# Kernel tuning notes

Measured on AMD Instinct MI355X. Metric: run time of the kernel, lower is better.

The kernel has to match this reference:

```python
import jax, jax.numpy as jnp
import numpy as np

D_MODEL = 1024
NUM_HEADS = 16
MAX_SEQ_LEN = 2048
BATCH = 4
SEQ_LEN = 2048


def setup_inputs() -> dict:
    key = jax.random.key(0)
    ks = jax.random.split(key, 7)
    s = 0.02
    return {
        "x": jax.random.normal(ks[0], (BATCH, SEQ_LEN, D_MODEL), dtype=jnp.float32),
        "Wq": jax.random.normal(ks[1], (D_MODEL, D_MODEL), dtype=jnp.float32) * s,
        "Wk": jax.random.normal(ks[2], (D_MODEL, D_MODEL), dtype=jnp.float32) * s,
        "Wv": jax.random.normal(ks[3], (D_MODEL, D_MODEL), dtype=jnp.float32) * s,
        "Wo": jax.random.normal(ks[4], (D_MODEL, D_MODEL), dtype=jnp.float32) * s,
        "bo": jnp.zeros((D_MODEL,), dtype=jnp.float32),
        "bias_table": jax.random.normal(ks[5], (2 * MAX_SEQ_LEN - 1, NUM_HEADS), dtype=jnp.float32) * s,
    }


def reference(x, Wq, Wk, Wv, Wo, bo, bias_table):
    B, S, D = x.shape
    H = NUM_HEADS
    hd = D // H
    scale = hd ** -0.5

    # torch Linear: y = x @ W.T
    q = (x @ Wq.T).reshape(B, S, H, hd).transpose(0, 2, 1, 3)  # [B,H,S,hd]
    k = (x @ Wk.T).reshape(B, S, H, hd).transpose(0, 2, 1, 3)
    v = (x @ Wv.T).reshape(B, S, H, hd).transpose(0, 2, 1, 3)

    scores = jnp.einsum("bhqd,bhkd->bhqk", q, k) * scale  # [B,H,S,S]

    # relative index: coords[:,None] - coords[None,:] + max_seq_len - 1
    coords = jnp.arange(S)
    rel_idx = coords[:, None] - coords[None, :] + MAX_SEQ_LEN - 1  # [S,S]
    rel_bias = bias_table[rel_idx]              # [S,S,H]
    rel_bias = rel_bias.transpose(2, 0, 1)[None]  # [1,H,S,S]

    probs = jax.nn.softmax(scores + rel_bias, axis=-1)
    ctx = jnp.einsum("bhqk,bhkd->bhqd", probs, v)  # [B,H,S,hd]
    ctx = ctx.transpose(0, 2, 1, 3).reshape(B, S, D)
    return ctx @ Wo.T + bo
```

## Files before the change

### kernel.cpp

```cpp
#include <hip/hip_runtime.h>
#include <string.h>

typedef unsigned short u16;
typedef unsigned int   u32;
typedef __attribute__((ext_vector_type(8))) short short8;
typedef __attribute__((ext_vector_type(4))) float f32x4;
typedef __attribute__((ext_vector_type(16))) float f32x16;
typedef __attribute__((ext_vector_type(2))) __fp16 h2;
typedef __attribute__((ext_vector_type(8))) __fp16 h8;
typedef __attribute__((ext_vector_type(2))) unsigned int u32x2;

__device__ __forceinline__ u16 f2b(float f) {
  u32 u = __float_as_uint(f);
  u32 r = (u + 0x7fffu + ((u >> 16) & 1u)) >> 16;
  return (u16)r;
}
__device__ __forceinline__ void cp16(const u16* g, u16* l) {
  __builtin_amdgcn_global_load_lds(
      (const __attribute__((address_space(1))) void*)g,
      (__attribute__((address_space(3))) void*)l, 16, 0, 0);
}
__device__ __forceinline__ void plswap(u32& a, u32& b) {
  u32x2 r = __builtin_amdgcn_permlane32_swap(a, b, false, false);
  a = r[0]; b = r[1];
}

__global__ __launch_bounds__(256) void cvt_f2b_kernel(const float* __restrict__ in,
                                                      u16* __restrict__ out, int n) {
  int i = (blockIdx.x * 256 + threadIdx.x) * 4;
  if (i + 3 < n) {
    float4 v = *(const float4*)&in[i];
    ushort4 o = make_ushort4(f2b(v.x), f2b(v.y), f2b(v.z), f2b(v.w));
    *(ushort4*)&out[i] = o;
  }
}
__global__ __launch_bounds__(256) void cvtw_kernel(const float* __restrict__ w0,
                                                   const float* __restrict__ w1,
                                                   const float* __restrict__ w2,
                                                   const float* __restrict__ w3,
                                                   u16* __restrict__ out) {
  const float* src = (blockIdx.y == 0) ? w0 : (blockIdx.y == 1) ? w1
                   : (blockIdx.y == 2) ? w2 : w3;
  int i = (blockIdx.x * 256 + threadIdx.x) * 4;
  float4 v = *(const float4*)&src[i];
  ushort4 o = make_ushort4(f2b(v.x), f2b(v.y), f2b(v.z), f2b(v.w));
  *(ushort4*)&out[(size_t)blockIdx.y * 1048576 + i] = o;
}

__global__ __launch_bounds__(256) void bias4x_kernel(const float* __restrict__ bt,
                                                     f32x4* __restrict__ gb4) {
  int idx = blockIdx.x * 256 + threadIdx.x;
  int h = idx >> 12, j = idx & 4095;
  f32x4 v;
  #pragma unroll
  for (int e = 0; e < 4; ++e) {
    int r = j - 3 + e;
    r = r < 0 ? 0 : (r > 4094 ? 4094 : r);
    v[e] = bt[r * 16 + h] * 1.44269504f;
  }
  gb4[idx] = v;
}

template<int MODE>
__global__ __launch_bounds__(256) void gemm128_bt(
    const u16* __restrict__ A, const u16* __restrict__ Bw,
    void* __restrict__ outp, const float* __restrict__ bias,
    const int M, const int N, const int K) {
  __shared__ __attribute__((aligned(16))) u16 As[2][128 * 32];
  __shared__ __attribute__((aligned(16))) u16 Bs[2][128 * 32];

  const u16* Bw2 = Bw;
  if (MODE == 0) Bw2 += ((size_t)blockIdx.z) << 20;

  const int tid  = threadIdx.x;
  const int wave = tid >> 6, lane = tid & 63;
  const int quad = lane >> 4, l15 = lane & 15;
  const int wm   = (wave >> 1) * 64, wn = (wave & 1) * 64;
  const int m0   = blockIdx.x * 128, n0 = blockIdx.y * 128;

  const int srow = wave * 32 + (lane >> 2);
  const int scol = (lane & 3) * 8;
  const u16* gA0 = A   + (size_t)(m0 + srow) * K + scol;
  const u16* gA1 = gA0 + (size_t)16 * K;
  const u16* gB0 = Bw2 + (size_t)(n0 + srow) * K + scol;
  const u16* gB1 = gB0 + (size_t)16 * K;
  const int lo0 = (wave * 32) * 32, lo1 = (wave * 32 + 16) * 32;

  cp16(gA0, &As[0][lo0]); cp16(gA1, &As[0][lo1]);
  cp16(gB0, &Bs[0][lo0]); cp16(gB1, &Bs[0][lo1]);
  gA0 += 32; gA1 += 32; gB0 += 32; gB1 += 32;

  f32x4 acc[4][4] = {};
  const int nk = K >> 5;
  for (int kt = 0; kt < nk; ++kt) {
    const int cur = kt & 1;
    __syncthreads();
    if (kt + 1 < nk) {
      cp16(gA0, &As[1 - cur][lo0]); cp16(gA1, &As[1 - cur][lo1]);
      cp16(gB0, &Bs[1 - cur][lo0]); cp16(gB1, &Bs[1 - cur][lo1]);
      gA0 += 32; gA1 += 32; gB0 += 32; gB1 += 32;
    }
    short8 af[4], bf[4];
    #pragma unroll
    for (int mi = 0; mi < 4; ++mi)
      af[mi] = *(const short8*)&As[cur][(wm + mi * 16 + l15) * 32 + quad * 8];
    #pragma unroll
    for (int ni = 0; ni < 4; ++ni)
      bf[ni] = *(const short8*)&Bs[cur][(wn + ni * 16 + l15) * 32 + quad * 8];
    #pragma unroll
    for (int mi = 0; mi < 4; ++mi)
      #pragma unroll
      for (int ni = 0; ni < 4; ++ni)
        acc[mi][ni] = __builtin_amdgcn_mfma_f32_16x16x32_bf16(af[mi], bf[ni], acc[mi][ni], 0, 0, 0);
  }

  #pragma unroll
  for (int mi = 0; mi < 4; ++mi)
    #pragma unroll
    for (int ni = 0; ni < 4; ++ni) {
      if (MODE == 0 && blockIdx.z == 2) {
        int mb = m0 + wm + mi * 16 + quad * 4;
        int n  = n0 + wn + ni * 16 + l15;
        int b = mb >> 11, s = mb & 2047, h = n >> 6, d = n & 63;
        u16* out = (u16*)outp + (((size_t)2) << 23);
        h2 p0 = __builtin_amdgcn_cvt_pkrtz(acc[mi][ni][0], acc[mi][ni][1]);
        h2 p1 = __builtin_amdgcn_cvt_pkrtz(acc[mi][ni][2], acc[mi][ni][3]);
        ushort4 o;
        memcpy(&o.x, &p0, 4);
        memcpy(&o.z, &p1, 4);
        *(ushort4*)&out[((((size_t)b * 16 + h) * 64 + d) << 11) + s] = o;
      } else {
        #pragma unroll
        for (int r = 0; r < 4; ++r) {
          int m = m0 + wm + mi * 16 + quad * 4 + r;
          int n = n0 + wn + ni * 16 + l15;
          float v = acc[mi][ni][r];
          if (MODE == 0) {
            int b = m >> 11, s = m & 2047, h = n >> 6, d = n & 63;
            u16* out = (u16*)outp + (((size_t)blockIdx.z) << 23);
            out[((((size_t)b * 16 + h) * 2048 + s) << 6) + d] = f2b(v);
          } else {
            ((float*)outp)[(size_t)m * N + n] = v + bias[n];
          }
        }
      }
    }
}

__global__ __launch_bounds__(256, 2) void attn_mfma_kernel(
    const u16* __restrict__ qb, const u16* __restrict__ kb, const u16* __restrict__ vtb,
    const f32x4* __restrict__ gb4, u16* __restrict__ ctx) {
  __shared__ __attribute__((aligned(16))) u16 Ks[2][64 * 64];
  __shared__ __attribute__((aligned(16))) u16 Vs[2][64 * 64];

  const int tid  = threadIdx.x;
  const int wave = tid >> 6, lane = tid & 63;
  const int l31  = lane & 31, hi = lane >> 5;
  const int xsw  = l31 & 7;
  const int bh   = blockIdx.x, h = bh & 15, b = bh >> 4;
  const int q0   = blockIdx.y * 256;

  short8 aQ[2][4];
  #pragma unroll
  for (int qs = 0; qs < 2; ++qs)
    #pragma unroll
    for (int ks = 0; ks < 4; ++ks)
      aQ[qs][ks] = *(const short8*)&qb[((size_t)bh * 2048 + q0 + wave * 64 + qs * 32 + l31) * 64
                                       + ks * 16 + hi * 8];

  f32x16 accO[2][2] = {};
  f32x16 accL[2]    = {};

  const h8 ones8 = {(__fp16)1.f, (__fp16)1.f, (__fp16)1.f, (__fp16)1.f,
                    (__fp16)1.f, (__fp16)1.f, (__fp16)1.f, (__fp16)1.f};

  const int krow = lane >> 3;
  const int kchk = (lane & 7) ^ krow;
  const u16* kbase = kb + (((size_t)bh * 2048) << 6);

  const int srow = tid >> 2, t0 = tid & 3, ssw = srow & 7;
  const u16* vrow = vtb + (((size_t)bh * 64 + srow) << 11) + t0 * 16;
  const int vo0 = srow * 64 + (((2 * t0    ) ^ ssw) << 3);
  const int vo1 = srow * 64 + (((2 * t0 + 1) ^ ssw) << 3);

  const f32x4* gb = gb4 + (h << 12);

  short8 vpre0 = *(const short8*)&vrow[0];
  short8 vpre1 = *(const short8*)&vrow[8];
  *(short8*)&Vs[0][vo0] = vpre0;
  *(short8*)&Vs[0][vo1] = vpre1;
  #pragma unroll
  for (int g = 0; g < 2; ++g)
    cp16(kbase + (size_t)(wave * 16 + g * 8 + krow) * 64 + kchk * 8,
         &Ks[0][(wave * 16 + g * 8) * 64]);
  vpre0 = *(const short8*)&vrow[64];
  vpre1 = *(const short8*)&vrow[72];

  for (int kt = 0; kt < 32; ++kt) {
    const int cur = kt & 1;
    __syncthreads();
    if (kt < 31) {
      #pragma unroll
      for (int g = 0; g < 2; ++g)
        cp16(kbase + (size_t)((kt + 1) * 64 + wave * 16 + g * 8 + krow) * 64 + kchk * 8,
             &Ks[1 - cur][(wave * 16 + g * 8) * 64]);
      *(short8*)&Vs[1 - cur][vo0] = vpre0;
      *(short8*)&Vs[1 - cur][vo1] = vpre1;
      if (kt < 30) {
        const u16* vp = vrow + ((size_t)(kt + 2) << 6);
        vpre0 = *(const short8*)&vp[0];
        vpre1 = *(const short8*)&vp[8];
      }
    }

    #pragma unroll
    for (int t = 0; t < 2; ++t) {
      short8 aK[4];
      #pragma unroll
      for (int ks = 0; ks < 4; ++ks)
        aK[ks] = *(const short8*)&Ks[cur][(t * 32 + l31) * 64
                                          + (((ks * 2 + hi) ^ xsw) << 3)];
      f32x16 accS[2] = {};
      __builtin_amdgcn_s_setprio(1);
      #pragma unroll
      for (int ks = 0; ks < 4; ++ks)
        #pragma unroll
        for (int qs = 0; qs < 2; ++qs)
          accS[qs] = __builtin_amdgcn_mfma_f32_32x32x16_bf16(aK[ks], aQ[qs][ks], accS[qs], 0, 0, 0);
      __builtin_amdgcn_s_setprio(0);

      u32 d[2][8];
      #pragma unroll
      for (int qs = 0; qs < 2; ++qs) {
        const int ibJ = q0 + wave * 64 + qs * 32 + l31 - kt * 64 - t * 32 - 4 * hi + 2047;
        #pragma unroll
        for (int rg = 0; rg < 4; ++rg) {
          const f32x4 bb4 = gb[ibJ - 8 * rg];
          float p0 = __builtin_amdgcn_exp2f(fmaf(accS[qs][4 * rg + 0], 0.18033688f, bb4[3]));
          float p1 = __builtin_amdgcn_exp2f(fmaf(accS[qs][4 * rg + 1], 0.18033688f, bb4[2]));
          float p2 = __builtin_amdgcn_exp2f(fmaf(accS[qs][4 * rg + 2], 0.18033688f, bb4[1]));
          float p3 = __builtin_amdgcn_exp2f(fmaf(accS[qs][4 * rg + 3], 0.18033688f, bb4[0]));
          h2 e0; e0[0] = (__fp16)p0; e0[1] = (__fp16)p1;
          h2 e1; e1[0] = (__fp16)p2; e1[1] = (__fp16)p3;
          memcpy(&d[qs][2 * rg],     &e0, 4);
          memcpy(&d[qs][2 * rg + 1], &e1, 4);
        }
      }

      #pragma unroll
      for (int sl = 0; sl < 2; ++sl) {
        const int ch = ((t * 2 + sl) * 2 + hi) ^ xsw;
        short8 av0 = *(const short8*)&Vs[cur][(     l31) * 64 + (ch << 3)];
        short8 av1 = *(const short8*)&Vs[cur][(32 + l31) * 64 + (ch << 3)];
        h8 avh0, avh1;
        memcpy(&avh0, &av0, 16);
        memcpy(&avh1, &av1, 16);
        __builtin_amdgcn_s_setprio(1);
        #pragma unroll
        for (int qs = 0; qs < 2; ++qs) {
          u32 F0 = d[qs][4 * sl], F1 = d[qs][4 * sl + 1];
          u32 F2 = d[qs][4 * sl + 2], F3 = d[qs][4 * sl + 3];
          plswap(F0, F2);
          plswap(F1, F3);
          union { u32 w[4]; h8 v; } uf;
          uf.w[0] = F0; uf.w[1] = F1; uf.w[2] = F2; uf.w[3] = F3;
          accO[qs][0] = __builtin_amdgcn_mfma_f32_32x32x16_f16(avh0, uf.v, accO[qs][0], 0, 0, 0);
          accO[qs][1] = __builtin_amdgcn_mfma_f32_32x32x16_f16(avh1, uf.v, accO[qs][1], 0, 0, 0);
          accL[qs]    = __builtin_amdgcn_mfma_f32_32x32x16_f16(ones8, uf.v, accL[qs], 0, 0, 0);
        }
        __builtin_amdgcn_s_setprio(0);
      }
    }
  }

  #pragma unroll
  for (int qs = 0; qs < 2; ++qs) {
    const float inv = 1.0f / accL[qs][0];
    const int q = q0 + wave * 64 + qs * 32 + l31;
    #pragma unroll
    for (int dt = 0; dt < 2; ++dt)
      #pragma unroll
      for (int rg = 0; rg < 4; ++rg) {
        ushort4 o = make_ushort4(f2b(accO[qs][dt][4 * rg + 0] * inv), f2b(accO[qs][dt][4 * rg + 1] * inv),
                                 f2b(accO[qs][dt][4 * rg + 2] * inv), f2b(accO[qs][dt][4 * rg + 3] * inv));
        *(ushort4*)&ctx[((size_t)b * 2048 + q) * 1024 + h * 64 + dt * 32 + rg * 8 + hi * 4] = o;
      }
  }
}

extern "C" void kernel_launch(void* const* d_in, const int* in_sizes, int n_in,
                              void* d_out, int out_size, void* d_ws, size_t ws_size,
                              hipStream_t stream) {
  const float* x          = (const float*)d_in[0];
  const float* Wq         = (const float*)d_in[1];
  const float* Wk         = (const float*)d_in[2];
  const float* Wv         = (const float*)d_in[3];
  const float* Wo         = (const float*)d_in[4];
  const float* bo         = (const float*)d_in[5];
  const float* bias_table = (const float*)d_in[6];
  float* out = (float*)d_out;

  char* ws = (char*)d_ws;
  u16* xb   = (u16*)(ws);
  u16* wqb  = (u16*)(ws + 16777216);
  u16* wob  = (u16*)(ws + 16777216 + 3 * 2097152);
  u16* qb   = (u16*)(ws + 25165824);
  u16* kb   = qb + 8388608;
  u16* vtb  = kb + 8388608;
  u16* ctxb = (u16*)(ws + 75497472);
  f32x4* gb4 = (f32x4*)(ws);

  cvt_f2b_kernel<<<8192, 256, 0, stream>>>(x, xb, 8388608);
  cvtw_kernel<<<dim3(1024, 4), 256, 0, stream>>>(Wq, Wk, Wv, Wo, wqb);

  gemm128_bt<0><<<dim3(64, 8, 3), 256, 0, stream>>>(
      xb, wqb, (void*)qb, nullptr, 8192, 1024, 1024);

  bias4x_kernel<<<256, 256, 0, stream>>>(bias_table, gb4);

  attn_mfma_kernel<<<dim3(64, 8), 256, 0, stream>>>(qb, kb, vtb, gb4, ctxb);

  gemm128_bt<1><<<dim3(64, 8), 256, 0, stream>>>(
      ctxb, wob, (void*)out, bo, 8192, 1024, 1024);
}
```

Baseline: 291.1 us.

## Stage relative-bias slice in LDS and merge conversion kernels into one launch

The attention kernel now copies the per-head, per-query-block slice of the expanded bias table (2304 f32x4 entries, about 36KB) into shared memory at block start. The softmax loop then reads bias from LDS instead of global memory. The x and weight fp32-to-bf16 conversion kernels are also merged into a single launch to save one launch. The bigger LDS footprint (about 68KB per block) may cut occupancy below the 2 blocks per CU hinted by launch bounds, and the upfront copy adds a prologue.

```diff
diff --git a/kernel.cpp b/kernel.cpp
--- a/kernel.cpp
+++ b/kernel.cpp
@@ -25,26 +25,25 @@
   a = r[0]; b = r[1];
 }
 
-__global__ __launch_bounds__(256) void cvt_f2b_kernel(const float* __restrict__ in,
-                                                      u16* __restrict__ out, int n) {
-  int i = (blockIdx.x * 256 + threadIdx.x) * 4;
-  if (i + 3 < n) {
-    float4 v = *(const float4*)&in[i];
-    ushort4 o = make_ushort4(f2b(v.x), f2b(v.y), f2b(v.z), f2b(v.w));
-    *(ushort4*)&out[i] = o;
-  }
-}
-__global__ __launch_bounds__(256) void cvtw_kernel(const float* __restrict__ w0,
-                                                   const float* __restrict__ w1,
-                                                   const float* __restrict__ w2,
-                                                   const float* __restrict__ w3,
-                                                   u16* __restrict__ out) {
-  const float* src = (blockIdx.y == 0) ? w0 : (blockIdx.y == 1) ? w1
-                   : (blockIdx.y == 2) ? w2 : w3;
-  int i = (blockIdx.x * 256 + threadIdx.x) * 4;
-  float4 v = *(const float4*)&src[i];
-  ushort4 o = make_ushort4(f2b(v.x), f2b(v.y), f2b(v.z), f2b(v.w));
-  *(ushort4*)&out[(size_t)blockIdx.y * 1048576 + i] = o;
+__global__ __launch_bounds__(256) void prep_kernel(
+    const float* __restrict__ x,
+    const float* __restrict__ w0, const float* __restrict__ w1,
+    const float* __restrict__ w2, const float* __restrict__ w3,
+    u16* __restrict__ xb, u16* __restrict__ wqb) {
+  int bid = blockIdx.x;
+  if (bid < 8192) {
+    int i = (bid * 256 + threadIdx.x) * 4;
+    float4 v = *(const float4*)&x[i];
+    *(ushort4*)&xb[i] = make_ushort4(f2b(v.x), f2b(v.y), f2b(v.z), f2b(v.w));
+  } else {
+    bid -= 8192;
+    const int wsel = bid >> 10;
+    const float* src = (wsel == 0) ? w0 : (wsel == 1) ? w1 : (wsel == 2) ? w2 : w3;
+    int i = ((bid & 1023) * 256 + threadIdx.x) * 4;
+    float4 v = *(const float4*)&src[i];
+    *(ushort4*)&wqb[((size_t)wsel << 20) + i] =
+        make_ushort4(f2b(v.x), f2b(v.y), f2b(v.z), f2b(v.w));
+  }
 }
 
 __global__ __launch_bounds__(256) void bias4x_kernel(const float* __restrict__ bt,
@@ -152,6 +151,7 @@
     const f32x4* __restrict__ gb4, u16* __restrict__ ctx) {
   __shared__ __attribute__((aligned(16))) u16 Ks[2][64 * 64];
   __shared__ __attribute__((aligned(16))) u16 Vs[2][64 * 64];
+  __shared__ __attribute__((aligned(16))) f32x4 bias4[2304];
 
   const int tid  = threadIdx.x;
   const int wave = tid >> 6, lane = tid & 63;
@@ -160,6 +160,14 @@
   const int bh   = blockIdx.x, h = bh & 15, b = bh >> 4;
   const int q0   = blockIdx.y * 256;
 
+  {
+    const f32x4* gbh = gb4 + (h << 12);
+    for (int i = tid; i < 2304; i += 256) {
+      int j = q0 + i + 3; if (j > 4095) j = 4095;
+      bias4[i] = gbh[j];
+    }
+  }
+
   short8 aQ[2][4];
   #pragma unroll
   for (int qs = 0; qs < 2; ++qs)
@@ -182,8 +190,6 @@
   const u16* vrow = vtb + (((size_t)bh * 64 + srow) << 11) + t0 * 16;
   const int vo0 = srow * 64 + (((2 * t0    ) ^ ssw) << 3);
   const int vo1 = srow * 64 + (((2 * t0 + 1) ^ ssw) << 3);
-
-  const f32x4* gb = gb4 + (h << 12);
 
   short8 vpre0 = *(const short8*)&vrow[0];
   short8 vpre1 = *(const short8*)&vrow[8];
@@ -232,10 +238,10 @@
       u32 d[2][8];
       #pragma unroll
       for (int qs = 0; qs < 2; ++qs) {
-        const int ibJ = q0 + wave * 64 + qs * 32 + l31 - kt * 64 - t * 32 - 4 * hi + 2047;
+        const int ib3 = wave * 64 + qs * 32 + l31 - kt * 64 - t * 32 - 4 * hi + 2044;
         #pragma unroll
         for (int rg = 0; rg < 4; ++rg) {
-          const f32x4 bb4 = gb[ibJ - 8 * rg];
+          const f32x4 bb4 = bias4[ib3 - 8 * rg];
           float p0 = __builtin_amdgcn_exp2f(fmaf(accS[qs][4 * rg + 0], 0.18033688f, bb4[3]));
           float p1 = __builtin_amdgcn_exp2f(fmaf(accS[qs][4 * rg + 1], 0.18033688f, bb4[2]));
           float p2 = __builtin_amdgcn_exp2f(fmaf(accS[qs][4 * rg + 2], 0.18033688f, bb4[1]));
@@ -310,8 +316,7 @@
   u16* ctxb = (u16*)(ws + 75497472);
   f32x4* gb4 = (f32x4*)(ws);
 
-  cvt_f2b_kernel<<<8192, 256, 0, stream>>>(x, xb, 8388608);
-  cvtw_kernel<<<dim3(1024, 4), 256, 0, stream>>>(Wq, Wk, Wv, Wo, wqb);
+  prep_kernel<<<12288, 256, 0, stream>>>(x, Wq, Wk, Wv, Wo, xb, wqb);
 
   gemm128_bt<0><<<dim3(64, 8, 3), 256, 0, stream>>>(
       xb, wqb, (void*)qb, nullptr, 8192, 1024, 1024);
```

Measured after the change: 278.2 us. -4.4%, faster.
